# Kernel optimization log

Measured on AMD Instinct MI355X. Metric: run time of the kernel, lower is better.

Reference implementation:

```python
import jax, jax.numpy as jnp
import numpy as np

B, E, T, H = 2, 1024, 2048, 16
DH = E // H


def _conv1x1(x, W, b, mask):
    # x: [B,C,T], W: [O,C], b: [O], mask: [B,1,T] (norm=False -> plain conv on masked input)
    x = x * mask
    return jnp.einsum('oc,bct->bot', W, x) + b[None, :, None]


def setup_inputs() -> dict:
    key = jax.random.key(0)
    ks = jax.random.split(key, 16)
    inp = {
        'q': jax.random.normal(ks[0], (B, E, T), jnp.float32),
        'k': jax.random.normal(ks[1], (B, E, T), jnp.float32),
        'v': jax.random.normal(ks[2], (B, E, T), jnp.float32),
        'query_mask': (jax.random.uniform(ks[3], (B, 1, T)) < 0.9).astype(jnp.float32),
        'key_mask': (jax.random.uniform(ks[4], (B, 1, T)) < 0.9).astype(jnp.float32),
        'value_mask': (jax.random.uniform(ks[5], (B, 1, T)) < 0.9).astype(jnp.float32),
        'Wq': jax.random.normal(ks[6], (E, E), jnp.float32) * (1.0 / np.sqrt(E)),
        'bq': jnp.zeros((E,), jnp.float32),
        'Wk': jax.random.normal(ks[7], (E, E), jnp.float32) * (1.0 / np.sqrt(E)),
        'bk': jnp.zeros((E,), jnp.float32),
        'Wv': jax.random.normal(ks[8], (E, E), jnp.float32) * (1.0 / np.sqrt(E)),
        'bv': jnp.zeros((E,), jnp.float32),
        'Wo': jax.random.normal(ks[9], (E, E), jnp.float32) * (1.0 / np.sqrt(E)),
        'bo': jnp.zeros((E,), jnp.float32),
    }
    return inp


def reference(q, k, v, query_mask, key_mask, value_mask, Wq, bq, Wk, bk, Wv, bv, Wo, bo):
    # 1x1 conv projections with input masking (norm=False path)
    qp = _conv1x1(q, Wq, bq, query_mask)   # [B,E,T]
    kp = _conv1x1(k, Wk, bk, key_mask)
    vp = _conv1x1(v, Wv, bv, value_mask)
    # split heads: [B,E,T] -> [B,H,DH,T]
    qh = qp.reshape(B, H, DH, T)
    kh = kp.reshape(B, H, DH, T)
    vh = vp.reshape(B, H, DH, T)
    # scores = q^T k with pre-softmax multiplicative masks, scaled by sqrt(embed_dim)
    scores = jnp.einsum('bhdq,bhdk->bhqk', qh, kh)
    scores = scores * query_mask[:, :, :, None] * key_mask[:, :, None, :] / np.sqrt(E)
    attn = jax.nn.softmax(scores, axis=-1) * key_mask[:, :, None, :]  # post-softmax mask
    # transpose_scores=False path: v @ scores (contracts v's time dim with the query dim)
    out = jnp.einsum('bhdq,bhqk->bhdk', vh, attn)  # [B,H,DH,T]
    out = out.reshape(B, E, T)
    return _conv1x1(out, Wo, bo, key_mask)
```

## Files before the change

### kernel.cpp

```cpp
#include <hip/hip_runtime.h>

#define B 2
#define E 1024
#define T 2048
#define H 16
#define DH 64

#define SCALE2 0.0450842200277801f

typedef _Float16 f16x8 __attribute__((ext_vector_type(8)));
typedef float f32x4 __attribute__((ext_vector_type(4)));
typedef float f32x16 __attribute__((ext_vector_type(16)));
typedef unsigned short ushort8v __attribute__((ext_vector_type(8)));
typedef unsigned int uint4v __attribute__((ext_vector_type(4)));

__device__ __forceinline__ f32x4 mfma16(f16x8 a, f16x8 b, f32x4 c) {
  return __builtin_amdgcn_mfma_f32_16x16x32_f16(a, b, c, 0, 0, 0);
}
__device__ __forceinline__ f32x16 mfma32(f16x8 a, f16x8 b, f32x16 c) {
  return __builtin_amdgcn_mfma_f32_32x32x16_f16(a, b, c, 0, 0, 0);
}
__device__ __forceinline__ unsigned short f16u(float x) {
  _Float16 h = (_Float16)x;
  return __builtin_bit_cast(unsigned short, h);
}
__device__ __forceinline__ float ex2(float x) {
  return __builtin_amdgcn_exp2f(x);
}
__device__ __forceinline__ unsigned int pk16(float a, float b) {
  auto h = __builtin_amdgcn_cvt_pkrtz(a, b);
  return __builtin_bit_cast(unsigned int, h);
}
__device__ __forceinline__ void plswap(unsigned int& a, unsigned int& b) {
  auto r = __builtin_amdgcn_permlane32_swap(a, b, false, false);
  a = r[0];
  b = r[1];
}

__global__ __launch_bounds__(256) void prep_weights(
    const float* __restrict__ Wq, const float* __restrict__ Wk,
    const float* __restrict__ Wv, const float* __restrict__ Wo,
    unsigned short* __restrict__ WqB, unsigned short* __restrict__ WkB,
    unsigned short* __restrict__ WvB, unsigned short* __restrict__ WoB) {
  const int which = blockIdx.y;
  const int i = (blockIdx.x * 256 + threadIdx.x) * 4;
  const float* src = which == 0 ? Wq : which == 1 ? Wk : which == 2 ? Wv : Wo;
  unsigned short* dst = which == 0 ? WqB : which == 1 ? WkB : which == 2 ? WvB : WoB;
  float4 v = *(const float4*)&src[i];
  ((unsigned int*)&dst[i])[0] = f16u(v.x) | ((unsigned)f16u(v.y) << 16);
  ((unsigned int*)&dst[i])[1] = f16u(v.z) | ((unsigned)f16u(v.w) << 16);
}

__global__ __launch_bounds__(256) void transpose_cvt(
    const float* __restrict__ q, const float* __restrict__ k,
    const float* __restrict__ v, unsigned short* __restrict__ XtQ,
    unsigned short* __restrict__ XtK, unsigned short* __restrict__ XtV) {
  __shared__ float Xs[32 * 36];
  const int z = blockIdx.z, which = z >> 1, b = z & 1;
  const float* X = which == 0 ? q : which == 1 ? k : v;
  unsigned short* O = which == 0 ? XtQ : which == 1 ? XtK : XtV;
  const int e0 = blockIdx.y * 32, t0 = blockIdx.x * 32;
  const int tid = threadIdx.x;
  const int r = tid >> 3, c = (tid & 7) * 4;
  *(float4*)&Xs[r * 36 + c] = *(const float4*)&X[((size_t)b * E + e0 + r) * T + t0 + c];
  __syncthreads();
  unsigned short h[4];
#pragma unroll
  for (int j = 0; j < 4; ++j) h[j] = f16u(Xs[(c + j) * 36 + r]);
  const size_t o = ((size_t)b * T + t0 + r) * E + e0 + c;
  ((unsigned int*)&O[o])[0] = h[0] | ((unsigned)h[1] << 16);
  ((unsigned int*)&O[o])[1] = h[2] | ((unsigned)h[3] << 16);
}

__global__ __launch_bounds__(256) void proj_qkv(
    const unsigned short* __restrict__ WqB, const unsigned short* __restrict__ WkB,
    const unsigned short* __restrict__ WvB, const unsigned short* __restrict__ XtQ,
    const unsigned short* __restrict__ XtK, const unsigned short* __restrict__ XtV,
    const float* __restrict__ bq, const float* __restrict__ bk,
    const float* __restrict__ bv, const float* __restrict__ qmask,
    const float* __restrict__ kmask, const float* __restrict__ vmask,
    unsigned short* __restrict__ qp2, unsigned short* __restrict__ kp2,
    unsigned short* __restrict__ vp2) {
  __shared__ unsigned short Ah[128 * 72], Bs[128 * 72];
  const int b = blockIdx.z, my = blockIdx.y;
  const int which = my >> 3, o0 = (my & 7) * 128, t0 = blockIdx.x * 128;
  const unsigned short* W = which == 0 ? WqB : which == 1 ? WkB : WvB;
  const unsigned short* Xt = which == 0 ? XtQ : which == 1 ? XtK : XtV;
  const float* bias = which == 0 ? bq : which == 1 ? bk : bv;
  const float* mask = which == 0 ? qmask : which == 1 ? kmask : vmask;

  const int tid = threadIdx.x, wave = tid >> 6, lane = tid & 63;
  const int lg = lane & 15, quad = lane >> 4;
  const int wm = (wave & 1) * 64, wn = (wave >> 1) * 64;
  const int sr = tid >> 3, sc = (tid & 7) * 8;

  f32x4 acc[4][4];
#pragma unroll
  for (int i = 0; i < 4; ++i)
#pragma unroll
    for (int j = 0; j < 4; ++j) acc[i][j] = (f32x4){0.f, 0.f, 0.f, 0.f};

  for (int k0 = 0; k0 < E; k0 += 64) {
    ushort8v ra[4], rb[4];
#pragma unroll
    for (int p = 0; p < 4; ++p) {
      ra[p] = *(const ushort8v*)&W[(size_t)(o0 + p * 32 + sr) * E + k0 + sc];
      rb[p] = *(const ushort8v*)&Xt[((size_t)b * T + t0 + p * 32 + sr) * E + k0 + sc];
    }
    __syncthreads();
#pragma unroll
    for (int p = 0; p < 4; ++p) {
      *(ushort8v*)&Ah[(p * 32 + sr) * 72 + sc] = ra[p];
      *(ushort8v*)&Bs[(p * 32 + sr) * 72 + sc] = rb[p];
    }
    __syncthreads();
    f16x8 af[4][2];
#pragma unroll
    for (int mt = 0; mt < 4; ++mt) {
      af[mt][0] = *(const f16x8*)&Ah[(wm + mt * 16 + lg) * 72 + quad * 8];
      af[mt][1] = *(const f16x8*)&Ah[(wm + mt * 16 + lg) * 72 + 32 + quad * 8];
    }
#pragma unroll
    for (int nt = 0; nt < 4; ++nt) {
      f16x8 b0 = *(const f16x8*)&Bs[(wn + nt * 16 + lg) * 72 + quad * 8];
      f16x8 b1 = *(const f16x8*)&Bs[(wn + nt * 16 + lg) * 72 + 32 + quad * 8];
#pragma unroll
      for (int mt = 0; mt < 4; ++mt) {
        f32x4 c = acc[mt][nt];
        c = mfma16(af[mt][0], b0, c);
        c = mfma16(af[mt][1], b1, c);
        acc[mt][nt] = c;
      }
    }
  }
#pragma unroll
  for (int nt = 0; nt < 4; ++nt) {
    const int tcol = t0 + wn + nt * 16 + lg;
    const float mv = mask[b * T + tcol];
#pragma unroll
    for (int mt = 0; mt < 4; ++mt) {
      const int oF = o0 + wm + mt * 16 + quad * 4;
      float v4[4];
      if (which == 0) {
        const float s = mv * SCALE2;
#pragma unroll
        for (int r = 0; r < 4; ++r) v4[r] = (acc[mt][nt][r] + bias[oF + r]) * s;
      } else if (which == 1) {
#pragma unroll
        for (int r = 0; r < 4; ++r) v4[r] = (acc[mt][nt][r] + bias[oF + r]) * mv;
      } else {
#pragma unroll
        for (int r = 0; r < 4; ++r) v4[r] = acc[mt][nt][r] * mv + bias[oF + r];
      }
      if (which <= 1) {
        unsigned short* O = which == 0 ? qp2 : kp2;
        const int head = (o0 + wm) >> 6;
        const int bh2 = b * H + head;
        const size_t idx8 =
            (((size_t)(bh2 * (T / 32) + (tcol >> 5)) * 4 + mt) * 32 + (tcol & 31)) * 2 +
            (quad >> 1);
        unsigned int* dst = (unsigned int*)(O + idx8 * 8 + (quad & 1) * 4);
        dst[0] = f16u(v4[0]) | ((unsigned)f16u(v4[1]) << 16);
        dst[1] = f16u(v4[2]) | ((unsigned)f16u(v4[3]) << 16);
      } else {
        const int head = (o0 + wm) >> 6;
        const int bh2 = b * H + head;
        const size_t qbase =
            ((size_t)(bh2 * (T / 16) + (tcol >> 4))) * 1024 + (tcol & 15);
#pragma unroll
        for (int r = 0; r < 4; ++r) {
          const int hd = (oF + r) & 63;
          vp2[qbase + ((size_t)(hd >> 5) * 32 + (hd & 31)) * 16] = f16u(v4[r]);
        }
      }
    }
  }
}

__global__ __launch_bounds__(256) void attn_stats(
    const unsigned short* __restrict__ qp2, const unsigned short* __restrict__ kp2,
    float* __restrict__ sPart) {
  const int bh = blockIdx.y;
  const int z = blockIdx.z;
  const int q0 = blockIdx.x * 128;
  const int tid = threadIdx.x, wave = tid >> 6, lane = tid & 63;
  const int ln = lane & 31, half = lane >> 5;

  const int t32q = (q0 >> 5) + wave;
  f16x8 aq[4];
#pragma unroll
  for (int s = 0; s < 4; ++s)
    aq[s] = *(const f16x8*)&qp2[((((size_t)bh * (T / 32) + t32q) * 4 + s) * 64 +
                                 ln * 2 + half) * 8];

  float lacc[16];
#pragma unroll
  for (int r = 0; r < 16; ++r) lacc[r] = 0.f;

  const int kbase = z * (T / 2);
  const int kend = kbase + T / 2;

  const unsigned short* pk0 =
      kp2 + (((size_t)bh * (T / 32) + (kbase >> 5)) * 4) * 512 + (ln * 2 + half) * 8;
  const unsigned short* pk1 = pk0 + 2048;

  f16x8 bkr[2][4];
#pragma unroll
  for (int s = 0; s < 4; ++s) {
    bkr[0][s] = *(const f16x8*)(pk0 + s * 512);
    bkr[1][s] = *(const f16x8*)(pk1 + s * 512);
  }
  pk0 += 4096;
  pk1 += 4096;

  for (int kt = kbase; kt < kend; kt += 64) {
    f16x8 nb[2][4];
#pragma unroll
    for (int s = 0; s < 4; ++s) {
      nb[0][s] = *(const f16x8*)(pk0 + s * 512);
      nb[1][s] = *(const f16x8*)(pk1 + s * 512);
    }
    pk0 += 4096;
    pk1 += 4096;
    f32x16 S0 = {}, S1 = {};
#pragma unroll
    for (int s = 0; s < 4; ++s) {
      S0 = mfma32(aq[s], bkr[0][s], S0);
      S1 = mfma32(aq[s], bkr[1][s], S1);
    }
#pragma unroll
    for (int r = 0; r < 16; ++r) lacc[r] += ex2(S0[r]) + ex2(S1[r]);
#pragma unroll
    for (int nt = 0; nt < 2; ++nt)
#pragma unroll
      for (int s = 0; s < 4; ++s) bkr[nt][s] = nb[nt][s];
  }
#pragma unroll
  for (int off = 1; off < 32; off <<= 1)
#pragma unroll
    for (int r = 0; r < 16; ++r) lacc[r] += __shfl_xor(lacc[r], off, 64);
  if (ln == 0) {
#pragma unroll
    for (int t = 0; t < 4; ++t) {
      f32x4 o;
#pragma unroll
      for (int j = 0; j < 4; ++j) o[j] = lacc[t * 4 + j];
      *(f32x4*)&sPart[((size_t)z * (B * H) + bh) * T + q0 + wave * 32 + t * 8 +
                      half * 4] = o;
    }
  }
}

__global__ __launch_bounds__(256) void stats_merge(
    const float* __restrict__ sPart, float* __restrict__ lLog) {
  const int i = (blockIdx.x * 256 + threadIdx.x) * 4;
  const int N = B * H * T;
  f32x4 a = *(const f32x4*)&sPart[i];
  f32x4 b = *(const f32x4*)&sPart[N + i];
  f32x4 o;
#pragma unroll
  for (int j = 0; j < 4; ++j) o[j] = -__builtin_amdgcn_logf(a[j] + b[j]);
  *(f32x4*)&lLog[i] = o;
}

#define APPLY_LOAD(AQ, AV, LL)                                                        \
  {                                                                                   \
    _Pragma("unroll") for (int s = 0; s < 4; ++s) AQ[s] =                             \
        *(const f16x8*)(pq + s * 512);                                                \
    _Pragma("unroll") for (int dt = 0; dt < 2; ++dt)                                  \
        _Pragma("unroll") for (int f = 0; f < 2; ++f) AV[dt][f] =                     \
        *(const f16x8*)(pv + dt * 512 + f * 1024);                                    \
    _Pragma("unroll") for (int t = 0; t < 4; ++t) LL[t] =                             \
        *(const f32x4*)(pl + t * 8);                                                  \
    pq += 2048;                                                                       \
    pv += 2048;                                                                       \
    pl += 32;                                                                         \
  }

#define APPLY_COMPUTE(AQ, AV, LL)                                                     \
  {                                                                                   \
    f32x16 S0, S1;                                                                    \
    _Pragma("unroll") for (int r = 0; r < 16; ++r) {                                  \
      const float c_ = LL[r >> 2][r & 3];                                             \
      S0[r] = c_;                                                                     \
      S1[r] = c_;                                                                     \
    }                                                                                 \
    _Pragma("unroll") for (int s = 0; s < 4; ++s) S0 = mfma32(AQ[s], bkk[0][s], S0);  \
    _Pragma("unroll") for (int s = 0; s < 4; ++s) S1 = mfma32(AQ[s], bkk[1][s], S1);  \
    {                                                                                 \
      unsigned int w[8];                                                              \
      _Pragma("unroll") for (int p = 0; p < 8; ++p)                                   \
          w[p] = pk16(ex2(S0[p * 2 + 0]), ex2(S0[p * 2 + 1]));                        \
      plswap(w[0], w[2]); plswap(w[1], w[3]);                                         \
      plswap(w[4], w[6]); plswap(w[5], w[7]);                                         \
      uint4v f0v, f1v;                                                                \
      f0v[0] = w[0]; f0v[1] = w[1]; f0v[2] = w[2]; f0v[3] = w[3];                     \
      f1v[0] = w[4]; f1v[1] = w[5]; f1v[2] = w[6]; f1v[3] = w[7];                     \
      const f16x8 pf0 = __builtin_bit_cast(f16x8, f0v);                               \
      const f16x8 pf1 = __builtin_bit_cast(f16x8, f1v);                               \
      acc00 = mfma32(AV[0][0], pf0, acc00);                                           \
      acc00 = mfma32(AV[0][1], pf1, acc00);                                           \
      acc01 = mfma32(AV[1][0], pf0, acc01);                                           \
      acc01 = mfma32(AV[1][1], pf1, acc01);                                           \
    }                                                                                 \
    {                                                                                 \
      unsigned int w[8];                                                              \
      _Pragma("unroll") for (int p = 0; p < 8; ++p)                                   \
          w[p] = pk16(ex2(S1[p * 2 + 0]), ex2(S1[p * 2 + 1]));                        \
      plswap(w[0], w[2]); plswap(w[1], w[3]);                                         \
      plswap(w[4], w[6]); plswap(w[5], w[7]);                                         \
      uint4v f0v, f1v;                                                                \
      f0v[0] = w[0]; f0v[1] = w[1]; f0v[2] = w[2]; f0v[3] = w[3];                     \
      f1v[0] = w[4]; f1v[1] = w[5]; f1v[2] = w[6]; f1v[3] = w[7];                     \
      const f16x8 pf0 = __builtin_bit_cast(f16x8, f0v);                               \
      const f16x8 pf1 = __builtin_bit_cast(f16x8, f1v);                               \
      acc10 = mfma32(AV[0][0], pf0, acc10);                                           \
      acc10 = mfma32(AV[0][1], pf1, acc10);                                           \
      acc11 = mfma32(AV[1][0], pf0, acc11);                                           \
      acc11 = mfma32(AV[1][1], pf1, acc11);                                           \
    }                                                                                 \
  }

__global__ __launch_bounds__(256) void attn_apply(
    const unsigned short* __restrict__ qp2, const unsigned short* __restrict__ kp2,
    const unsigned short* __restrict__ vp2, const float* __restrict__ lLog,
    unsigned short* __restrict__ ao) {
  __shared__ float st[64 * 130];
  const int n = blockIdx.x;
  const int s_ = n >> 3;
  const int bh = (n & 7) * 4 + (s_ >> 4);
  const int kblk = (s_ & 15) * 128;
  const int b = bh >> 4, h = bh & 15;
  const int tid = threadIdx.x, wave = tid >> 6, lane = tid & 63;
  const int ln = lane & 31, half = lane >> 5;
  const int kt = wave & 1, qh = wave >> 1;

  const int t32k = (kblk >> 5) + kt * 2;
  f16x8 bkk[2][4];
#pragma unroll
  for (int sub = 0; sub < 2; ++sub)
#pragma unroll
    for (int s = 0; s < 4; ++s)
      bkk[sub][s] = *(const f16x8*)&kp2[((((size_t)bh * (T / 32) + t32k + sub) * 4 + s) *
                                             64 + ln * 2 + half) * 8];

  f32x16 acc00 = {}, acc01 = {}, acc10 = {}, acc11 = {};
  const int qstart = qh * (T / 2);
  const int qend = qstart + T / 2;

  const unsigned short* pq =
      qp2 + (((size_t)bh * (T / 32) + (qstart >> 5)) * 4) * 512 + (ln * 2 + half) * 8;
  const unsigned short* pv =
      vp2 + ((size_t)bh * (T / 16) + (qstart >> 4)) * 1024 + ln * 16 + half * 8;
  const float* pl = lLog + (size_t)bh * T + qstart + half * 4;

  f16x8 aqX[4], avX[2][2], aqY[4], avY[2][2];
  f32x4 llX[4], llY[4];
  APPLY_LOAD(aqX, avX, llX)

  for (int qt = qstart; qt < qend; qt += 64) {
    APPLY_LOAD(aqY, avY, llY)
    APPLY_COMPUTE(aqX, avX, llX)
    APPLY_LOAD(aqX, avX, llX)
    APPLY_COMPUTE(aqY, avY, llY)
  }

  __syncthreads();
  if (qh == 1) {
#pragma unroll
    for (int i = 0; i < 16; ++i) {
      st[(0 * 16 + i) * 130 + kt * 65 + lane] = acc00[i];
      st[(1 * 16 + i) * 130 + kt * 65 + lane] = acc01[i];
      st[(2 * 16 + i) * 130 + kt * 65 + lane] = acc10[i];
      st[(3 * 16 + i) * 130 + kt * 65 + lane] = acc11[i];
    }
  }
  __syncthreads();
  if (qh == 0) {
#pragma unroll
    for (int i = 0; i < 16; ++i) {
      acc00[i] += st[(0 * 16 + i) * 130 + kt * 65 + lane];
      acc01[i] += st[(1 * 16 + i) * 130 + kt * 65 + lane];
      acc10[i] += st[(2 * 16 + i) * 130 + kt * 65 + lane];
      acc11[i] += st[(3 * 16 + i) * 130 + kt * 65 + lane];
    }
#pragma unroll
    for (int sub = 0; sub < 2; ++sub) {
      const int kcol = kblk + kt * 64 + sub * 32 + ln;
      const size_t obase = ((size_t)b * T + kcol) * E + h * DH;
#pragma unroll
      for (int dt = 0; dt < 2; ++dt) {
        const float* a = sub == 0 ? (dt ? (const float*)&acc01 : (const float*)&acc00)
                                  : (dt ? (const float*)&acc11 : (const float*)&acc10);
#pragma unroll
        for (int t = 0; t < 4; ++t) {
          uint2 wv;
          wv.x = f16u(a[t * 4 + 0]) | ((unsigned)f16u(a[t * 4 + 1]) << 16);
          wv.y = f16u(a[t * 4 + 2]) | ((unsigned)f16u(a[t * 4 + 3]) << 16);
          *(uint2*)&ao[obase + dt * 32 + t * 8 + half * 4] = wv;
        }
      }
    }
  }
}

__global__ __launch_bounds__(256) void proj_final(
    const unsigned short* __restrict__ WoB, const unsigned short* __restrict__ ao,
    const float* __restrict__ bo, const float* __restrict__ kmask,
    float* __restrict__ out) {
  __shared__ unsigned short As[64 * 68], Bs[128 * 68];
  const int b = blockIdx.z, o0 = blockIdx.y * 64, t0 = blockIdx.x * 128;
  const int tid = threadIdx.x, wave = tid >> 6, lane = tid & 63;
  const int ln = lane & 31, half = lane >> 5;
  const int wn = wave * 32;
  const int ar = tid >> 2, ac = (tid & 3) * 16;
  const int br = tid >> 1, bc = (tid & 1) * 32;

  f32x16 acc0 = {}, acc1 = {};

  for (int k0 = 0; k0 < E; k0 += 64) {
    ushort8v a0 = *(const ushort8v*)&WoB[(size_t)(o0 + ar) * E + k0 + ac];
    ushort8v a1 = *(const ushort8v*)&WoB[(size_t)(o0 + ar) * E + k0 + ac + 8];
    ushort8v b0 = *(const ushort8v*)&ao[((size_t)b * T + t0 + br) * E + k0 + bc];
    ushort8v b1 = *(const ushort8v*)&ao[((size_t)b * T + t0 + br) * E + k0 + bc + 8];
    ushort8v b2 = *(const ushort8v*)&ao[((size_t)b * T + t0 + br) * E + k0 + bc + 16];
    ushort8v b3 = *(const ushort8v*)&ao[((size_t)b * T + t0 + br) * E + k0 + bc + 24];
    __syncthreads();
    *(ushort8v*)&As[ar * 68 + ac] = a0;
    *(ushort8v*)&As[ar * 68 + ac + 8] = a1;
    *(ushort8v*)&Bs[br * 68 + bc] = b0;
    *(ushort8v*)&Bs[br * 68 + bc + 8] = b1;
    *(ushort8v*)&Bs[br * 68 + bc + 16] = b2;
    *(ushort8v*)&Bs[br * 68 + bc + 24] = b3;
    __syncthreads();
#pragma unroll
    for (int s = 0; s < 4; ++s) {
      f16x8 af0 = *(const f16x8*)&As[ln * 68 + s * 16 + half * 8];
      f16x8 af1 = *(const f16x8*)&As[(32 + ln) * 68 + s * 16 + half * 8];
      f16x8 bf = *(const f16x8*)&Bs[(wn + ln) * 68 + s * 16 + half * 8];
      acc0 = mfma32(af0, bf, acc0);
      acc1 = mfma32(af1, bf, acc1);
    }
  }
  const int tcol = t0 + wn + ln;
  const float mv = kmask[b * T + tcol];
#pragma unroll
  for (int dt = 0; dt < 2; ++dt) {
    const float* a = dt ? (const float*)&acc1 : (const float*)&acc0;
#pragma unroll
    for (int t = 0; t < 4; ++t)
#pragma unroll
      for (int j = 0; j < 4; ++j) {
        const int e = o0 + dt * 32 + t * 8 + half * 4 + j;
        out[((size_t)b * E + e) * T + tcol] = a[t * 4 + j] * mv + bo[e];
      }
  }
}

extern "C" void kernel_launch(void* const* d_in, const int* in_sizes, int n_in,
                              void* d_out, int out_size, void* d_ws, size_t ws_size,
                              hipStream_t stream) {
  const float* q = (const float*)d_in[0];
  const float* k = (const float*)d_in[1];
  const float* v = (const float*)d_in[2];
  const float* qmask = (const float*)d_in[3];
  const float* kmask = (const float*)d_in[4];
  const float* vmask = (const float*)d_in[5];
  const float* Wq = (const float*)d_in[6];
  const float* bq = (const float*)d_in[7];
  const float* Wk = (const float*)d_in[8];
  const float* bk = (const float*)d_in[9];
  const float* Wv = (const float*)d_in[10];
  const float* bv = (const float*)d_in[11];
  const float* Wo = (const float*)d_in[12];
  const float* bo = (const float*)d_in[13];

  char* w = (char*)d_ws;
  const size_t WB = (size_t)E * E * sizeof(unsigned short);
  const size_t TB = (size_t)B * T * E * sizeof(unsigned short);
  unsigned short* WqB = (unsigned short*)(w + 0 * WB);
  unsigned short* WkB = (unsigned short*)(w + 1 * WB);
  unsigned short* WvB = (unsigned short*)(w + 2 * WB);
  unsigned short* WoB = (unsigned short*)(w + 3 * WB);
  size_t off = 4 * WB;
  unsigned short* XtQ = (unsigned short*)(w + off); off += TB;
  unsigned short* qp2 = (unsigned short*)(w + off); off += TB;
  unsigned short* kp2 = (unsigned short*)(w + off); off += TB;
  unsigned short* vp2 = (unsigned short*)(w + off); off += TB;
  float* lLog = (float*)(w + off); off += (size_t)B * H * T * sizeof(float);
  float* sPart = (float*)(w + off); off += (size_t)2 * B * H * T * sizeof(float);
  unsigned short* XtK = (unsigned short*)(w + off); off += TB;
  unsigned short* XtV = (unsigned short*)(w + off); off += TB;
  unsigned short* ao = XtQ;

  dim3 bl(256);
  prep_weights<<<dim3((E * E) / 1024, 4), bl, 0, stream>>>(
      Wq, Wk, Wv, Wo, WqB, WkB, WvB, WoB);
  transpose_cvt<<<dim3(T / 32, E / 32, 3 * B), bl, 0, stream>>>(
      q, k, v, XtQ, XtK, XtV);
  proj_qkv<<<dim3(T / 128, 24, B), bl, 0, stream>>>(
      WqB, WkB, WvB, XtQ, XtK, XtV, bq, bk, bv, qmask, kmask, vmask, qp2, kp2, vp2);
  attn_stats<<<dim3(T / 128, B * H, 2), bl, 0, stream>>>(qp2, kp2, sPart);
  stats_merge<<<dim3((B * H * T) / 1024), bl, 0, stream>>>(sPart, lLog);
  attn_apply<<<dim3(512), bl, 0, stream>>>(qp2, kp2, vp2, lLog, ao);
  proj_final<<<dim3(T / 128, E / 64, B), bl, 0, stream>>>(
      WoB, ao, bo, kmask, (float*)d_out);
}
```

Before: 256.0 us.

## Write attention output in MFMA fragment layout and drop LDS staging in output projection

attn_apply now stores its output in a pre-swizzled fragment layout that matches the B-operand of the 32x32x16 MFMA. This lets proj_final load fragments straight from global memory, so its shared-memory tiles and both barriers per k-step are gone. WoB fragments are also read directly from global memory. The cost is that reuse now relies on caches instead of LDS: each wave reloads the weight rows separately and loses cooperative coalesced staging.

```diff
diff --git a/kernel.cpp b/kernel.cpp
--- a/kernel.cpp
+++ b/kernel.cpp
@@ -324,7 +324,7 @@
 __global__ __launch_bounds__(256) void attn_apply(
     const unsigned short* __restrict__ qp2, const unsigned short* __restrict__ kp2,
     const unsigned short* __restrict__ vp2, const float* __restrict__ lLog,
-    unsigned short* __restrict__ ao) {
+    unsigned short* __restrict__ aoF) {
   __shared__ float st[64 * 130];
   const int n = blockIdx.x;
   const int s_ = n >> 3;
@@ -387,7 +387,7 @@
 #pragma unroll
     for (int sub = 0; sub < 2; ++sub) {
       const int kcol = kblk + kt * 64 + sub * 32 + ln;
-      const size_t obase = ((size_t)b * T + kcol) * E + h * DH;
+      const size_t fbase = ((size_t)b * (T / 32) + (kcol >> 5)) * 64 + h * 4;
 #pragma unroll
       for (int dt = 0; dt < 2; ++dt) {
         const float* a = sub == 0 ? (dt ? (const float*)&acc01 : (const float*)&acc00)
@@ -397,7 +397,8 @@
           uint2 wv;
           wv.x = f16u(a[t * 4 + 0]) | ((unsigned)f16u(a[t * 4 + 1]) << 16);
           wv.y = f16u(a[t * 4 + 2]) | ((unsigned)f16u(a[t * 4 + 3]) << 16);
-          *(uint2*)&ao[obase + dt * 32 + t * 8 + half * 4] = wv;
+          const int s = dt * 2 + (t >> 1);
+          *(uint2*)&aoF[(fbase + s) * 512 + (ln * 2 + (t & 1)) * 8 + half * 4] = wv;
         }
       }
     }
@@ -405,39 +406,28 @@
 }
 
 __global__ __launch_bounds__(256) void proj_final(
-    const unsigned short* __restrict__ WoB, const unsigned short* __restrict__ ao,
+    const unsigned short* __restrict__ WoB, const unsigned short* __restrict__ aoF,
     const float* __restrict__ bo, const float* __restrict__ kmask,
     float* __restrict__ out) {
-  __shared__ unsigned short As[64 * 68], Bs[128 * 68];
   const int b = blockIdx.z, o0 = blockIdx.y * 64, t0 = blockIdx.x * 128;
   const int tid = threadIdx.x, wave = tid >> 6, lane = tid & 63;
   const int ln = lane & 31, half = lane >> 5;
   const int wn = wave * 32;
-  const int ar = tid >> 2, ac = (tid & 3) * 16;
-  const int br = tid >> 1, bc = (tid & 1) * 32;
+  const int tt = (t0 + wn) >> 5;
 
   f32x16 acc0 = {}, acc1 = {};
 
+  const unsigned short* pa0 = WoB + (size_t)(o0 + ln) * E + half * 8;
+  const unsigned short* pa1 = WoB + (size_t)(o0 + 32 + ln) * E + half * 8;
+  const unsigned short* pb =
+      aoF + ((size_t)b * (T / 32) + tt) * 64 * 512 + (ln * 2 + half) * 8;
+
   for (int k0 = 0; k0 < E; k0 += 64) {
-    ushort8v a0 = *(const ushort8v*)&WoB[(size_t)(o0 + ar) * E + k0 + ac];
-    ushort8v a1 = *(const ushort8v*)&WoB[(size_t)(o0 + ar) * E + k0 + ac + 8];
-    ushort8v b0 = *(const ushort8v*)&ao[((size_t)b * T + t0 + br) * E + k0 + bc];
-    ushort8v b1 = *(const ushort8v*)&ao[((size_t)b * T + t0 + br) * E + k0 + bc + 8];
-    ushort8v b2 = *(const ushort8v*)&ao[((size_t)b * T + t0 + br) * E + k0 + bc + 16];
-    ushort8v b3 = *(const ushort8v*)&ao[((size_t)b * T + t0 + br) * E + k0 + bc + 24];
-    __syncthreads();
-    *(ushort8v*)&As[ar * 68 + ac] = a0;
-    *(ushort8v*)&As[ar * 68 + ac + 8] = a1;
-    *(ushort8v*)&Bs[br * 68 + bc] = b0;
-    *(ushort8v*)&Bs[br * 68 + bc + 8] = b1;
-    *(ushort8v*)&Bs[br * 68 + bc + 16] = b2;
-    *(ushort8v*)&Bs[br * 68 + bc + 24] = b3;
-    __syncthreads();
 #pragma unroll
     for (int s = 0; s < 4; ++s) {
-      f16x8 af0 = *(const f16x8*)&As[ln * 68 + s * 16 + half * 8];
-      f16x8 af1 = *(const f16x8*)&As[(32 + ln) * 68 + s * 16 + half * 8];
-      f16x8 bf = *(const f16x8*)&Bs[(wn + ln) * 68 + s * 16 + half * 8];
+      f16x8 af0 = *(const f16x8*)(pa0 + k0 + s * 16);
+      f16x8 af1 = *(const f16x8*)(pa1 + k0 + s * 16);
+      f16x8 bf = *(const f16x8*)(pb + (size_t)((k0 >> 4) + s) * 512);
       acc0 = mfma32(af0, bf, acc0);
       acc1 = mfma32(af1, bf, acc1);
     }
@@ -491,7 +481,7 @@
   float* sPart = (float*)(w + off); off += (size_t)2 * B * H * T * sizeof(float);
   unsigned short* XtK = (unsigned short*)(w + off); off += TB;
   unsigned short* XtV = (unsigned short*)(w + off); off += TB;
-  unsigned short* ao = XtQ;
+  unsigned short* aoF = XtQ;
 
   dim3 bl(256);
   prep_weights<<<dim3((E * E) / 1024, 4), bl, 0, stream>>>(
@@ -502,7 +492,7 @@
       WqB, WkB, WvB, XtQ, XtK, XtV, bq, bk, bv, qmask, kmask, vmask, qp2, kp2, vp2);
   attn_stats<<<dim3(T / 128, B * H, 2), bl, 0, stream>>>(qp2, kp2, sPart);
   stats_merge<<<dim3((B * H * T) / 1024), bl, 0, stream>>>(sPart, lLog);
-  attn_apply<<<dim3(512), bl, 0, stream>>>(qp2, kp2, vp2, lLog, ao);
+  attn_apply<<<dim3(512), bl, 0, stream>>>(qp2, kp2, vp2, lLog, aoF);
   proj_final<<<dim3(T / 128, E / 64, B), bl, 0, stream>>>(
-      WoB, ao, bo, kmask, (float*)d_out);
-}
+      WoB, aoF, bo, kmask, (float*)d_out);
+}
```

Result: slower. 282.1 us (+10.2%).
